# Kernel optimization log

Hardware: AMD Instinct MI355X
Metric: run time of the kernel (lower is better)

The kernel has to match this reference:

```python
import jax, jax.numpy as jnp
import numpy as np

COARSE_BINS = 256
XMIN = 0.0
XMAX = 1.0


def setup_inputs() -> dict:
    key = jax.random.key(0)
    k1, k2 = jax.random.split(key)
    inputs = jax.random.normal(k1, (4096, COARSE_BINS, 2), dtype=jnp.float32)
    x = jax.random.uniform(k2, (4096, 4096), dtype=jnp.float32)
    return {"inputs": inputs, "x": x}


def _coarse_positions(params0):
    # params0: [B, coarse_bins] -- the per-bin position offsets (inputs[..., 0])
    bin_width = (XMAX - XMIN) / COARSE_BINS
    centers = jnp.linspace(XMIN + bin_width / 2, XMAX - bin_width / 2, COARSE_BINS)
    x_abs = centers[None, :] + jnp.tanh(params0) * 0.5 * bin_width
    return jnp.clip(x_abs, XMIN, XMAX)  # monotone non-decreasing per row


def reference(inputs, x):
    # inputs: [B, coarse_bins, 2], x: [B, Nq]
    x_abs = _coarse_positions(inputs[..., 0])  # [B, coarse_bins]
    t_values = inputs[..., 1]                  # [B, coarse_bins]
    interp1 = lambda xi, xc, yc: jnp.interp(
        xi, xc, yc, left="extrapolate", right="extrapolate"
    )
    return jax.vmap(interp1)(x, x_abs, t_values)  # [B, Nq]
```

## Files before the change

### kernel.cpp

```cpp
#include <hip/hip_runtime.h>
#include <math.h>

#define NBINS 256
#define BINW (1.0f / 256.0f)

__global__ __launch_bounds__(256) void pwl_kernel(
    const float* __restrict__ inp,
    const float* __restrict__ x,
    float* __restrict__ out,
    int nq)
{
    __shared__ float2 s_xt[NBINS];

    const int b   = blockIdx.x;
    const int tid = threadIdx.x;

    float2 p = ((const float2*)inp)[(size_t)b * NBINS + tid];
    float center = ((float)tid + 0.5f) * BINW;
    float xa = center + tanhf(p.x) * (0.5f * BINW);
    xa = fminf(fmaxf(xa, 0.0f), 1.0f);
    s_xt[tid] = make_float2(xa, p.y);
    __syncthreads();

    const float4* xrow = (const float4*)(x + (size_t)b * nq);
    float4*       orow = (float4*)(out + (size_t)b * nq);
    const int nvec = nq >> 2;

    for (int i = tid; i < nvec; i += 256) {
        float4 q = xrow[i];
        float4 r;
        float* qv = (float*)&q;
        float* rv = (float*)&r;
#pragma unroll
        for (int c = 0; c < 4; ++c) {
            float xi = qv[c];
            int k = (int)(xi * 256.0f);
            k = min(max(k, 0), NBINS - 1);

            float2 pk = s_xt[k];
            int o = (xi >= pk.x) ? (k + 1) : (k - 1);
            if (o < 0)        o = 1;
            if (o > NBINS-1)  o = NBINS - 2;

            float2 po = s_xt[o];
            float2 lo = (o > k) ? pk : po;
            float2 hi = (o > k) ? po : pk;

            rv[c] = lo.y + (xi - lo.x) * ((hi.y - lo.y) / (hi.x - lo.x));
        }
        orow[i] = r;
    }
}

extern "C" void kernel_launch(void* const* d_in, const int* in_sizes, int n_in,
                              void* d_out, int out_size, void* d_ws, size_t ws_size,
                              hipStream_t stream)
{
    const float* inp = (const float*)d_in[0];
    const float* x   = (const float*)d_in[1];
    float*       out = (float*)d_out;

    const int B  = in_sizes[0] / (2 * NBINS);
    const int nq = in_sizes[1] / B;

    pwl_kernel<<<B, 256, 0, stream>>>(inp, x, out, nq);
}
```

Measured before the change: 26.85 us.

## Precompute slopes in LDS, batch four nontemporal vector loads per thread

Splits the shared table into separate x, t and slope arrays, with slopes computed once per row, so each query needs a single FMA instead of a divide. The main loop is unrolled to issue four independent 16-byte loads per thread before computing, which raises memory-level parallelism, and it uses nontemporal loads and stores to stream data without polluting the cache. The cost is an extra barrier and more LDS reads per query, three scalar loads instead of two float2 loads. The slope form can also differ slightly numerically from the reference interpolation.

```diff
diff --git a/kernel.cpp b/kernel.cpp
--- a/kernel.cpp
+++ b/kernel.cpp
@@ -2,7 +2,8 @@
 #include <math.h>
 
 #define NBINS 256
-#define BINW (1.0f / 256.0f)
+
+typedef float fx4 __attribute__((ext_vector_type(4)));
 
 __global__ __launch_bounds__(256) void pwl_kernel(
     const float* __restrict__ inp,
@@ -10,45 +11,63 @@
     float* __restrict__ out,
     int nq)
 {
-    __shared__ float2 s_xt[NBINS];
+    __shared__ float s_x[NBINS];
+    __shared__ float s_t[NBINS];
+    __shared__ float s_m[NBINS];
 
     const int b   = blockIdx.x;
     const int tid = threadIdx.x;
 
     float2 p = ((const float2*)inp)[(size_t)b * NBINS + tid];
-    float center = ((float)tid + 0.5f) * BINW;
-    float xa = center + tanhf(p.x) * (0.5f * BINW);
+    float xa = ((float)tid + 0.5f) * (1.0f / 256.0f)
+             + tanhf(p.x) * (0.5f / 256.0f);
     xa = fminf(fmaxf(xa, 0.0f), 1.0f);
-    s_xt[tid] = make_float2(xa, p.y);
+    s_x[tid] = xa;
+    s_t[tid] = p.y;
+    __syncthreads();
+    if (tid < NBINS - 1) {
+        s_m[tid] = (s_t[tid + 1] - s_t[tid]) / (s_x[tid + 1] - s_x[tid]);
+    }
     __syncthreads();
 
-    const float4* xrow = (const float4*)(x + (size_t)b * nq);
-    float4*       orow = (float4*)(out + (size_t)b * nq);
+    auto evalf = [&](float xi) -> float {
+        int k = (int)(xi * 256.0f);
+        k = min(max(k, 0), NBINS - 1);
+        float xk = s_x[k];
+        int s = (xi >= xk) ? k : k - 1;
+        s = min(max(s, 0), NBINS - 2);
+        return fmaf(xi - s_x[s], s_m[s], s_t[s]);
+    };
+    auto eval4 = [&](fx4 q) -> fx4 {
+        fx4 r;
+        r.x = evalf(q.x); r.y = evalf(q.y);
+        r.z = evalf(q.z); r.w = evalf(q.w);
+        return r;
+    };
+
+    const fx4* xrow = (const fx4*)(x + (size_t)b * nq);
+    fx4*       orow = (fx4*)(out + (size_t)b * nq);
     const int nvec = nq >> 2;
 
-    for (int i = tid; i < nvec; i += 256) {
-        float4 q = xrow[i];
-        float4 r;
-        float* qv = (float*)&q;
-        float* rv = (float*)&r;
-#pragma unroll
-        for (int c = 0; c < 4; ++c) {
-            float xi = qv[c];
-            int k = (int)(xi * 256.0f);
-            k = min(max(k, 0), NBINS - 1);
-
-            float2 pk = s_xt[k];
-            int o = (xi >= pk.x) ? (k + 1) : (k - 1);
-            if (o < 0)        o = 1;
-            if (o > NBINS-1)  o = NBINS - 2;
-
-            float2 po = s_xt[o];
-            float2 lo = (o > k) ? pk : po;
-            float2 hi = (o > k) ? po : pk;
-
-            rv[c] = lo.y + (xi - lo.x) * ((hi.y - lo.y) / (hi.x - lo.x));
-        }
-        orow[i] = r;
+    int i = tid;
+    for (; i + 768 < nvec; i += 1024) {
+        fx4 q0 = __builtin_nontemporal_load(&xrow[i]);
+        fx4 q1 = __builtin_nontemporal_load(&xrow[i + 256]);
+        fx4 q2 = __builtin_nontemporal_load(&xrow[i + 512]);
+        fx4 q3 = __builtin_nontemporal_load(&xrow[i + 768]);
+        fx4 r0 = eval4(q0);
+        fx4 r1 = eval4(q1);
+        fx4 r2 = eval4(q2);
+        fx4 r3 = eval4(q3);
+        __builtin_nontemporal_store(r0, &orow[i]);
+        __builtin_nontemporal_store(r1, &orow[i + 256]);
+        __builtin_nontemporal_store(r2, &orow[i + 512]);
+        __builtin_nontemporal_store(r3, &orow[i + 768]);
+    }
+    for (; i < nvec; i += 256) {
+        fx4 q = __builtin_nontemporal_load(&xrow[i]);
+        fx4 r = eval4(q);
+        __builtin_nontemporal_store(r, &orow[i]);
     }
 }
 
```

Result: slower. 27.57 us (+2.7%).

## Precompute per-knot slopes, process two rows per block with hoisted nontemporal loads

Applied to the files above, without the earlier changes.

Each block now handles two rows and holds a shared table of knot position, value, and left/right slopes, so every query needs one LDS read and one FMA instead of two reads and a divide. All eight float4 query loads are issued before the table build, so global latency overlaps the tanh work, and loads and stores use nontemporal hints. The code hardcodes nq=4096 (four vectors per thread per row) and an even batch size, so other shapes would break. Redundant neighbour knot computation adds a small amount of setup work.

```diff
diff --git a/kernel.cpp b/kernel.cpp
--- a/kernel.cpp
+++ b/kernel.cpp
@@ -2,7 +2,14 @@
 #include <math.h>
 
 #define NBINS 256
-#define BINW (1.0f / 256.0f)
+
+typedef float fx4 __attribute__((ext_vector_type(4)));
+
+
+__device__ __forceinline__ float knot_pos(int j, float p0) {
+    float xa = ((float)j + 0.5f) * (1.0f / 256.0f) + tanhf(p0) * (0.5f / 256.0f);
+    return fminf(fmaxf(xa, 0.0f), 1.0f);
+}
 
 __global__ __launch_bounds__(256) void pwl_kernel(
     const float* __restrict__ inp,
@@ -10,46 +17,68 @@
     float* __restrict__ out,
     int nq)
 {
-    __shared__ float2 s_xt[NBINS];
+    __shared__ fx4 s_tab[2][NBINS];
 
-    const int b   = blockIdx.x;
     const int tid = threadIdx.x;
+    const int r0  = blockIdx.x * 2;
+    const int r1  = r0 + 1;
 
-    float2 p = ((const float2*)inp)[(size_t)b * NBINS + tid];
-    float center = ((float)tid + 0.5f) * BINW;
-    float xa = center + tanhf(p.x) * (0.5f * BINW);
-    xa = fminf(fmaxf(xa, 0.0f), 1.0f);
-    s_xt[tid] = make_float2(xa, p.y);
+    const fx4* xrow0 = (const fx4*)(x + (size_t)r0 * nq);
+    const fx4* xrow1 = (const fx4*)(x + (size_t)r1 * nq);
+    fx4*       orow0 = (fx4*)(out + (size_t)r0 * nq);
+    fx4*       orow1 = (fx4*)(out + (size_t)r1 * nq);
+
+    fx4 q0 = __builtin_nontemporal_load(&xrow0[tid]);
+    fx4 q1 = __builtin_nontemporal_load(&xrow0[tid + 256]);
+    fx4 q2 = __builtin_nontemporal_load(&xrow0[tid + 512]);
+    fx4 q3 = __builtin_nontemporal_load(&xrow0[tid + 768]);
+    fx4 q4 = __builtin_nontemporal_load(&xrow1[tid]);
+    fx4 q5 = __builtin_nontemporal_load(&xrow1[tid + 256]);
+    fx4 q6 = __builtin_nontemporal_load(&xrow1[tid + 512]);
+    fx4 q7 = __builtin_nontemporal_load(&xrow1[tid + 768]);
+
+    const int im1 = max(tid - 1, 0);
+    const int ip1 = min(tid + 1, NBINS - 1);
+#pragma unroll
+    for (int rr = 0; rr < 2; ++rr) {
+        const float2* prow = (const float2*)(inp + ((size_t)r0 + rr) * (2 * NBINS));
+        float2 pm = prow[im1], pc = prow[tid], pp = prow[ip1];
+        float xm = knot_pos(im1, pm.x);
+        float xc = knot_pos(tid, pc.x);
+        float xp = knot_pos(ip1, pp.x);
+        float mL = (pc.y - pm.y) / (xc - xm);
+        float mH = (pp.y - pc.y) / (xp - xc);
+        fx4 e;
+        e.x = xc;
+        e.y = pc.y;
+        e.z = (tid > 0)         ? mL : mH;
+        e.w = (tid < NBINS - 1) ? mH : mL;
+        s_tab[rr][tid] = e;
+    }
     __syncthreads();
 
-    const float4* xrow = (const float4*)(x + (size_t)b * nq);
-    float4*       orow = (float4*)(out + (size_t)b * nq);
-    const int nvec = nq >> 2;
+    auto evalf = [&](int rr, float xi) -> float {
+        int k = (int)(xi * 256.0f);
+        k = min(max(k, 0), NBINS - 1);
+        fx4 e = s_tab[rr][k];
+        float m = (xi >= e.x) ? e.w : e.z;
+        return fmaf(xi - e.x, m, e.y);
+    };
+    auto eval4 = [&](int rr, fx4 q) -> fx4 {
+        fx4 r;
+        r.x = evalf(rr, q.x); r.y = evalf(rr, q.y);
+        r.z = evalf(rr, q.z); r.w = evalf(rr, q.w);
+        return r;
+    };
 
-    for (int i = tid; i < nvec; i += 256) {
-        float4 q = xrow[i];
-        float4 r;
-        float* qv = (float*)&q;
-        float* rv = (float*)&r;
-#pragma unroll
-        for (int c = 0; c < 4; ++c) {
-            float xi = qv[c];
-            int k = (int)(xi * 256.0f);
-            k = min(max(k, 0), NBINS - 1);
-
-            float2 pk = s_xt[k];
-            int o = (xi >= pk.x) ? (k + 1) : (k - 1);
-            if (o < 0)        o = 1;
-            if (o > NBINS-1)  o = NBINS - 2;
-
-            float2 po = s_xt[o];
-            float2 lo = (o > k) ? pk : po;
-            float2 hi = (o > k) ? po : pk;
-
-            rv[c] = lo.y + (xi - lo.x) * ((hi.y - lo.y) / (hi.x - lo.x));
-        }
-        orow[i] = r;
-    }
+    __builtin_nontemporal_store(eval4(0, q0), &orow0[tid]);
+    __builtin_nontemporal_store(eval4(0, q1), &orow0[tid + 256]);
+    __builtin_nontemporal_store(eval4(0, q2), &orow0[tid + 512]);
+    __builtin_nontemporal_store(eval4(0, q3), &orow0[tid + 768]);
+    __builtin_nontemporal_store(eval4(1, q4), &orow1[tid]);
+    __builtin_nontemporal_store(eval4(1, q5), &orow1[tid + 256]);
+    __builtin_nontemporal_store(eval4(1, q6), &orow1[tid + 512]);
+    __builtin_nontemporal_store(eval4(1, q7), &orow1[tid + 768]);
 }
 
 extern "C" void kernel_launch(void* const* d_in, const int* in_sizes, int n_in,
@@ -63,5 +92,5 @@
     const int B  = in_sizes[0] / (2 * NBINS);
     const int nq = in_sizes[1] / B;
 
-    pwl_kernel<<<B, 256, 0, stream>>>(inp, x, out, nq);
+    pwl_kernel<<<B / 2, 256, 0, stream>>>(inp, x, out, nq);
 }
```

Result: no change. 27.38 us (+2.0%).
